# Kernel optimization log

Measured on AMD Instinct MI355X. Metric: run time of the kernel, lower is better.

The kernel has to match this reference:

```python
import jax, jax.numpy as jnp
import numpy as np

N_NODES = 100000   # ntoken
D = 128            # ninp
N_EDGES = 1600000  # n_nodes * avg_degree(16)


def setup_inputs() -> dict:
    key = jax.random.key(0)
    k0, k1, k2, k3 = jax.random.split(key, 4)
    # nn.Embedding weight, xavier_normal_ init; row 0 is padding_idx -> zeros
    emb = jax.random.normal(k0, (N_NODES, D), jnp.float32) * np.float32(np.sqrt(2.0 / (N_NODES + D)))
    emb = emb.at[0].set(0.0)
    # GCNConv weights (glorot) and biases (zeros), as in torch_geometric defaults
    W1 = jax.random.normal(k1, (D, 2 * D), jnp.float32) * np.float32(np.sqrt(2.0 / (D + 2 * D)))
    b1 = jnp.zeros((2 * D,), jnp.float32)
    W2 = jax.random.normal(k2, (2 * D, D), jnp.float32) * np.float32(np.sqrt(2.0 / (2 * D + D)))
    b2 = jnp.zeros((D,), jnp.float32)
    edge_index = jax.random.randint(k3, (2, N_EDGES), 0, N_NODES, dtype=jnp.int64)
    return {"emb": emb, "W1": W1, "b1": b1, "W2": W2, "b2": b2, "edge_index": edge_index}


def gcn_conv(x, W, b, src, dst, n):
    """torch_geometric GCNConv: add self-loops, sym deg^{-1/2} norm, edge_weight=1."""
    h = x @ W  # [n, out]
    loop = jnp.arange(n, dtype=src.dtype)
    src2 = jnp.concatenate([src, loop])
    dst2 = jnp.concatenate([dst, loop])
    # degree computed at destination (col) including self-loops
    deg = jax.ops.segment_sum(jnp.ones_like(src2, dtype=h.dtype), dst2, num_segments=n)
    dinv = jnp.where(deg > 0, jax.lax.rsqrt(deg), 0.0)
    norm = dinv[src2] * dinv[dst2]  # [E+n]
    msg = h[src2] * norm[:, None]   # gather + scale (memory-bound)
    out = jax.ops.segment_sum(msg, dst2, num_segments=n)  # scatter-add
    return out + b


def reference(emb, W1, b1, W2, b2, edge_index):
    src, dst = edge_index[0], edge_index[1]
    n = emb.shape[0]
    h = gcn_conv(emb, W1, b1, src, dst, n)   # [N, 2D]; dropout = identity (eval)
    out = gcn_conv(h, W2, b2, src, dst, n)   # [N, D]
    return out
```

## Files before the change

### kernel.cpp

```cpp
#include <hip/hip_runtime.h>

static constexpr int D = 128;
static constexpr int CAP = 64;
static constexpr int NSLICE = 8;

typedef __attribute__((ext_vector_type(8))) short bf16x8;
typedef __attribute__((ext_vector_type(4))) float f32x4;

__device__ inline unsigned bf16rne(float f) {
  unsigned u = __float_as_uint(f);
  return (u + 0x7FFFu + ((u >> 16) & 1u)) >> 16;
}

__global__ __launch_bounds__(256) void k_fill(const int* __restrict__ src,
                                              const int* __restrict__ dst,
                                              int* __restrict__ cnt,
                                              int* __restrict__ ell, int e, int n) {
  const int slice = blockIdx.x % NSLICE;
  const int chunk = blockIdx.x / NSLICE;
  const int lo = (int)((long long)n * slice / NSLICE);
  const int hi = (int)((long long)n * (slice + 1) / NSLICE);
  const int cbase = chunk * 4096;

  #pragma unroll
  for (int i = 0; i < 4; ++i) {
    int idx = cbase + i * 1024 + (int)threadIdx.x * 4;
    if (idx + 4 <= e) {
      int4 d4 = *(const int4*)(dst + idx);
      int4 s4 = *(const int4*)(src + idx);
      if (d4.x >= lo && d4.x < hi) { int p = atomicAdd(&cnt[d4.x], 1); if (p < CAP) ell[(size_t)d4.x * CAP + p] = s4.x; }
      if (d4.y >= lo && d4.y < hi) { int p = atomicAdd(&cnt[d4.y], 1); if (p < CAP) ell[(size_t)d4.y * CAP + p] = s4.y; }
      if (d4.z >= lo && d4.z < hi) { int p = atomicAdd(&cnt[d4.z], 1); if (p < CAP) ell[(size_t)d4.z * CAP + p] = s4.z; }
      if (d4.w >= lo && d4.w < hi) { int p = atomicAdd(&cnt[d4.w], 1); if (p < CAP) ell[(size_t)d4.w * CAP + p] = s4.w; }
    } else {
      for (int k = idx; k < e && k < idx + 4; ++k) {
        int s = src[k], d = dst[k];
        if (d >= lo && d < hi) { int p = atomicAdd(&cnt[d], 1); if (p < CAP) ell[(size_t)d * CAP + p] = s; }
      }
    }
  }
}

__global__ void k_cvt(const float4* __restrict__ in, uint2* __restrict__ out, int n4) {
  int i = blockIdx.x * blockDim.x + threadIdx.x;
  if (i >= n4) return;
  float4 v = in[i];
  uint2 r;
  r.x = bf16rne(v.x) | (bf16rne(v.y) << 16);
  r.y = bf16rne(v.z) | (bf16rne(v.w) << 16);
  out[i] = r;
}

__global__ void k_w1w2(const float* __restrict__ W1, const float* __restrict__ W2,
                       const float* __restrict__ b1, float* __restrict__ W,
                       float* __restrict__ c2) {
  int r = blockIdx.x, c = threadIdx.x;
  float acc = 0.f;
  for (int k = 0; k < 256; ++k) acc = fmaf(W1[r * 256 + k], W2[k * D + c], acc);
  W[r * D + c] = acc;
  if (r == 0) {
    float a2 = 0.f;
    for (int k = 0; k < 256; ++k) a2 = fmaf(b1[k], W2[k * D + c], a2);
    c2[c] = a2;
  }
}

__global__ void k_pack(const float* __restrict__ Wc, uint4* __restrict__ Wp) {
  int t = blockIdx.x * blockDim.x + threadIdx.x;
  if (t >= 2048) return;
  int l = t & 63, g = t >> 6;
  int ct = g >> 2, ks = g & 3;
  int col = ct * 16 + (l & 15);
  int k0 = ks * 32 + (l >> 4) * 8;
  unsigned r[4];
  #pragma unroll
  for (int jj = 0; jj < 4; ++jj) {
    unsigned lo = bf16rne(Wc[(size_t)(k0 + 2 * jj) * D + col]);
    unsigned hi = bf16rne(Wc[(size_t)(k0 + 2 * jj + 1) * D + col]);
    r[jj] = lo | (hi << 16);
  }
  Wp[t] = make_uint4(r[0], r[1], r[2], r[3]);
}

template<bool AOUT>
__global__ __launch_bounds__(256) void k_agg16(const uint2* __restrict__ x,
                                               const int* __restrict__ cnt,
                                               const int* __restrict__ ell,
                                               uint2* __restrict__ y,
                                               float* __restrict__ aout, int n) {
  int t = blockIdx.x * blockDim.x + threadIdx.x;
  int node = t >> 5, lane = t & 31;
  if (node >= n) return;
  int deg = cnt[node];
  float dd = rsqrtf(1.0f + (float)deg);
  int m = deg < CAP ? deg : CAP;
  const int* row = ell + (size_t)node * CAP;

  uint2 q = x[(size_t)node * 32 + lane];
  float4 acc;
  acc.x = __uint_as_float(q.x << 16) * dd;
  acc.y = __uint_as_float(q.x & 0xFFFF0000u) * dd;
  acc.z = __uint_as_float(q.y << 16) * dd;
  acc.w = __uint_as_float(q.y & 0xFFFF0000u) * dd;
  float ws = 0.f;

#define ACC4(Q, W)                                                         \
  acc.x = fmaf(__uint_as_float((Q).x << 16), (W), acc.x);                  \
  acc.y = fmaf(__uint_as_float((Q).x & 0xFFFF0000u), (W), acc.y);          \
  acc.z = fmaf(__uint_as_float((Q).y << 16), (W), acc.z);                  \
  acc.w = fmaf(__uint_as_float((Q).y & 0xFFFF0000u), (W), acc.w)

  int j = 0;
  for (; j + 8 <= m; j += 8) {
    int4 i0 = *(const int4*)(row + j);
    int4 i1 = *(const int4*)(row + j + 4);
    uint2 q0 = x[(size_t)i0.x * 32 + lane];
    uint2 q1 = x[(size_t)i0.y * 32 + lane];
    uint2 q2 = x[(size_t)i0.z * 32 + lane];
    uint2 q3 = x[(size_t)i0.w * 32 + lane];
    uint2 q4 = x[(size_t)i1.x * 32 + lane];
    uint2 q5 = x[(size_t)i1.y * 32 + lane];
    uint2 q6 = x[(size_t)i1.z * 32 + lane];
    uint2 q7 = x[(size_t)i1.w * 32 + lane];
    float w0 = rsqrtf(1.0f + (float)cnt[i0.x]);
    float w1 = rsqrtf(1.0f + (float)cnt[i0.y]);
    float w2 = rsqrtf(1.0f + (float)cnt[i0.z]);
    float w3 = rsqrtf(1.0f + (float)cnt[i0.w]);
    float w4 = rsqrtf(1.0f + (float)cnt[i1.x]);
    float w5 = rsqrtf(1.0f + (float)cnt[i1.y]);
    float w6 = rsqrtf(1.0f + (float)cnt[i1.z]);
    float w7 = rsqrtf(1.0f + (float)cnt[i1.w]);
    if (AOUT) ws += w0 + w1 + w2 + w3 + w4 + w5 + w6 + w7;
    ACC4(q0, w0); ACC4(q1, w1); ACC4(q2, w2); ACC4(q3, w3);
    ACC4(q4, w4); ACC4(q5, w5); ACC4(q6, w6); ACC4(q7, w7);
  }
  for (; j < m; ++j) {
    int s0 = row[j];
    uint2 q0 = x[(size_t)s0 * 32 + lane];
    float w0 = rsqrtf(1.0f + (float)cnt[s0]);
    if (AOUT) ws += w0;
    ACC4(q0, w0);
  }
#undef ACC4

  uint2 o;
  o.x = bf16rne(acc.x * dd) | (bf16rne(acc.y * dd) << 16);
  o.y = bf16rne(acc.z * dd) | (bf16rne(acc.w * dd) << 16);
  y[(size_t)node * 32 + lane] = o;
  if (AOUT && lane == 0) aout[node] = dd * (dd + ws);
}

__global__ __launch_bounds__(256) void k_gemm_mfma(const ushort* __restrict__ X,
                                                   const uint4* __restrict__ Wp,
                                                   const float* __restrict__ c2,
                                                   const float* __restrict__ b2,
                                                   const float* __restrict__ a,
                                                   float* __restrict__ Y, int n) {
  const int wv = threadIdx.x >> 6;
  const int l = threadIdx.x & 63;
  const int row0 = blockIdx.x * 64 + wv * 16;
  const int rA = row0 + (l & 15);
  const int kb = l >> 4;

  bf16x8 afr[4];
  #pragma unroll
  for (int ks = 0; ks < 4; ++ks) {
    bf16x8 z = 0;
    afr[ks] = (rA < n) ? *reinterpret_cast<const bf16x8*>(X + (size_t)rA * D + ks * 32 + kb * 8) : z;
  }

  float ar[4];
  #pragma unroll
  for (int r = 0; r < 4; ++r) {
    int row = row0 + kb * 4 + r;
    ar[r] = (row < n) ? a[row] : 0.f;
  }

  #pragma unroll
  for (int ct = 0; ct < 8; ++ct) {
    f32x4 acc = {0.f, 0.f, 0.f, 0.f};
    #pragma unroll
    for (int ks = 0; ks < 4; ++ks) {
      bf16x8 bfr = *reinterpret_cast<const bf16x8*>(Wp + (size_t)(ct * 4 + ks) * 64 + l);
      acc = __builtin_amdgcn_mfma_f32_16x16x32_bf16(afr[ks], bfr, acc, 0, 0, 0);
    }
    int col = ct * 16 + (l & 15);
    float cb = c2[col], bb = b2[col];
    #pragma unroll
    for (int r = 0; r < 4; ++r) {
      int row = row0 + kb * 4 + r;
      if (row < n) Y[(size_t)row * D + col] = acc[r] + ar[r] * cb + bb;
    }
  }
}

extern "C" void kernel_launch(void* const* d_in, const int* in_sizes, int n_in,
                              void* d_out, int out_size, void* d_ws, size_t ws_size,
                              hipStream_t stream) {
  const float* emb = (const float*)d_in[0];
  const float* W1  = (const float*)d_in[1];
  const float* b1  = (const float*)d_in[2];
  const float* W2  = (const float*)d_in[3];
  const float* b2  = (const float*)d_in[4];
  const int*   ei  = (const int*)d_in[5];

  const int n = in_sizes[0] / D;
  const int e = in_sizes[5] / 2;
  const int* src = ei;
  const int* dst = ei + e;

  const int B = 256;

  char* ws = (char*)d_ws;
  size_t off = 0;
  auto alloc = [&](size_t bytes) { void* p = ws + off; off = (off + bytes + 255) & ~(size_t)255; return p; };
  int*   cnt = (int*)  alloc((size_t)n * 4);
  int*   ell = (int*)  alloc((size_t)n * CAP * 4);
  float* Wc  = (float*)alloc((size_t)D * D * 4);
  uint4* Wp  = (uint4*)alloc(2048 * 16);
  float* c2  = (float*)alloc((size_t)D * 4);
  float* av  = (float*)alloc((size_t)n * 4);
  uint2* E16 = (uint2*)alloc((size_t)n * 32 * 8);
  uint2* S16 = (uint2*)alloc((size_t)n * 32 * 8);
  uint2* S2  = (uint2*)alloc((size_t)n * 32 * 8);
  float* out = (float*)d_out;

  (void)hipMemsetAsync(cnt, 0, (size_t)n * 4, stream);
  {
    int nchunk = (e + 4095) / 4096;
    k_fill<<<nchunk * NSLICE, B, 0, stream>>>(src, dst, cnt, ell, e, n);
  }

  {
    int n4 = n * 32;
    k_cvt<<<(n4 + B - 1) / B, B, 0, stream>>>((const float4*)emb, E16, n4);
  }

  k_w1w2<<<D, D, 0, stream>>>(W1, W2, b1, Wc, c2);
  k_pack<<<8, B, 0, stream>>>(Wc, Wp);

  {
    long long t = (long long)n * 32;
    k_agg16<false><<<(int)((t + B - 1) / B), B, 0, stream>>>(E16, cnt, ell, S16, nullptr, n);
  }
  {
    long long t = (long long)n * 32;
    k_agg16<true><<<(int)((t + B - 1) / B), B, 0, stream>>>(S16, cnt, ell, S2, av, n);
  }
  {
    int nblk = (n + 63) / 64;
    k_gemm_mfma<<<nblk, B, 0, stream>>>((const ushort*)S2, Wp, c2, b2, av, out, n);
  }
}
```

Baseline: 268.8 us.

## Bucket edges by destination slice in LDS and fuse prep kernels

Replaces the sliced ELL fill, which read every edge once per slice (8x), with a two-pass scheme. One pass bins each edge into per-slice queues in shared memory and writes them out as packed (local dst, src) words. A second kernel fills the ELL rows from each slice's queue. The bf16 conversion, W1·W2 product/packing and bias precompute are folded into the same launch, removing several kernel launches and the intermediate Wc buffer. Risks: bucket overflow drops edges if a chunk exceeds BCAP per slice, the 17-bit src packing caps node counts, and the extra queue traffic costs memory bandwidth.

```diff
diff --git a/kernel.cpp b/kernel.cpp
--- a/kernel.cpp
+++ b/kernel.cpp
@@ -3,6 +3,8 @@
 static constexpr int D = 128;
 static constexpr int CAP = 64;
 static constexpr int NSLICE = 8;
+static constexpr int BCAP = 768;
+static constexpr int CHUNK = 4096;
 
 typedef __attribute__((ext_vector_type(8))) short bf16x8;
 typedef __attribute__((ext_vector_type(4))) float f32x4;
@@ -12,74 +14,129 @@
   return (u + 0x7FFFu + ((u >> 16) & 1u)) >> 16;
 }
 
-__global__ __launch_bounds__(256) void k_fill(const int* __restrict__ src,
-                                              const int* __restrict__ dst,
-                                              int* __restrict__ cnt,
-                                              int* __restrict__ ell, int e, int n) {
+__global__ __launch_bounds__(256) void k_prep(
+    const int* __restrict__ src, const int* __restrict__ dst,
+    const float4* __restrict__ emb, uint2* __restrict__ E16,
+    const float* __restrict__ W1, const float* __restrict__ W2,
+    const float* __restrict__ b1, uint4* __restrict__ Wp, float* __restrict__ c2,
+    unsigned* __restrict__ queue, int* __restrict__ qtail,
+    int e, int q, int qcap, int nchunk, int ncvt, int n4) {
+  const int bid = blockIdx.x;
+  const int tid = threadIdx.x;
+
+  if (bid < nchunk) {
+    __shared__ unsigned buck[NSLICE][BCAP];
+    __shared__ int bcnt[NSLICE];
+    __shared__ int gbase[NSLICE];
+    if (tid < NSLICE) bcnt[tid] = 0;
+    __syncthreads();
+    const int base = bid * CHUNK;
+    #pragma unroll
+    for (int i = 0; i < 4; ++i) {
+      int idx = base + i * 1024 + tid * 4;
+      if (idx + 4 <= e) {
+        int4 d4 = *(const int4*)(dst + idx);
+        int4 s4 = *(const int4*)(src + idx);
+        { int d = d4.x, s = s4.x; int sl = d / q; int p = atomicAdd(&bcnt[sl], 1);
+          if (p < BCAP) buck[sl][p] = ((unsigned)(d - sl * q) << 17) | (unsigned)s; }
+        { int d = d4.y, s = s4.y; int sl = d / q; int p = atomicAdd(&bcnt[sl], 1);
+          if (p < BCAP) buck[sl][p] = ((unsigned)(d - sl * q) << 17) | (unsigned)s; }
+        { int d = d4.z, s = s4.z; int sl = d / q; int p = atomicAdd(&bcnt[sl], 1);
+          if (p < BCAP) buck[sl][p] = ((unsigned)(d - sl * q) << 17) | (unsigned)s; }
+        { int d = d4.w, s = s4.w; int sl = d / q; int p = atomicAdd(&bcnt[sl], 1);
+          if (p < BCAP) buck[sl][p] = ((unsigned)(d - sl * q) << 17) | (unsigned)s; }
+      } else {
+        for (int k = idx; k < e && k < idx + 4; ++k) {
+          int d = dst[k], s = src[k]; int sl = d / q; int p = atomicAdd(&bcnt[sl], 1);
+          if (p < BCAP) buck[sl][p] = ((unsigned)(d - sl * q) << 17) | (unsigned)s;
+        }
+      }
+    }
+    __syncthreads();
+    if (tid < NSLICE) {
+      int c = bcnt[tid] < BCAP ? bcnt[tid] : BCAP;
+      bcnt[tid] = c;
+      gbase[tid] = atomicAdd(&qtail[tid], c);
+    }
+    __syncthreads();
+    for (int s = 0; s < NSLICE; ++s) {
+      int cs = bcnt[s], gb = gbase[s];
+      unsigned* qs = queue + (size_t)s * qcap;
+      for (int i2 = tid; i2 < cs; i2 += 256) {
+        int pos = gb + i2;
+        if (pos < qcap) __builtin_nontemporal_store(buck[s][i2], qs + pos);
+      }
+    }
+  } else if (bid < nchunk + ncvt) {
+    int i0 = (bid - nchunk) * 1024 + tid;
+    #pragma unroll
+    for (int k = 0; k < 4; ++k) {
+      int i = i0 + k * 256;
+      if (i < n4) {
+        float4 v = emb[i];
+        uint2 r;
+        r.x = bf16rne(v.x) | (bf16rne(v.y) << 16);
+        r.y = bf16rne(v.z) | (bf16rne(v.w) << 16);
+        E16[i] = r;
+      }
+    }
+  } else {
+    int cb = bid - nchunk - ncvt;
+    if (cb < 8) {
+      int t = cb * 256 + tid;
+      int l = t & 63, g = t >> 6;
+      int ct = g >> 2, ks = g & 3;
+      int col = ct * 16 + (l & 15);
+      int k0 = ks * 32 + (l >> 4) * 8;
+      unsigned r[4];
+      #pragma unroll
+      for (int jj = 0; jj < 4; ++jj) {
+        float lo = 0.f, hi = 0.f;
+        for (int m = 0; m < 256; ++m) {
+          float w2v = W2[(size_t)m * D + col];
+          lo = fmaf(W1[(size_t)(k0 + 2 * jj) * 256 + m], w2v, lo);
+          hi = fmaf(W1[(size_t)(k0 + 2 * jj + 1) * 256 + m], w2v, hi);
+        }
+        r[jj] = bf16rne(lo) | (bf16rne(hi) << 16);
+      }
+      Wp[t] = make_uint4(r[0], r[1], r[2], r[3]);
+    } else if (tid < D) {
+      float a2 = 0.f;
+      for (int m = 0; m < 256; ++m) a2 = fmaf(b1[m], W2[(size_t)m * D + tid], a2);
+      c2[tid] = a2;
+    }
+  }
+}
+
+__global__ __launch_bounds__(256) void k_fillB(const unsigned* __restrict__ queue,
+                                               const int* __restrict__ qtail,
+                                               int* __restrict__ cnt,
+                                               int* __restrict__ ell, int q, int qcap) {
   const int slice = blockIdx.x % NSLICE;
   const int chunk = blockIdx.x / NSLICE;
-  const int lo = (int)((long long)n * slice / NSLICE);
-  const int hi = (int)((long long)n * (slice + 1) / NSLICE);
-  const int cbase = chunk * 4096;
-
-  #pragma unroll
-  for (int i = 0; i < 4; ++i) {
-    int idx = cbase + i * 1024 + (int)threadIdx.x * 4;
-    if (idx + 4 <= e) {
-      int4 d4 = *(const int4*)(dst + idx);
-      int4 s4 = *(const int4*)(src + idx);
-      if (d4.x >= lo && d4.x < hi) { int p = atomicAdd(&cnt[d4.x], 1); if (p < CAP) ell[(size_t)d4.x * CAP + p] = s4.x; }
-      if (d4.y >= lo && d4.y < hi) { int p = atomicAdd(&cnt[d4.y], 1); if (p < CAP) ell[(size_t)d4.y * CAP + p] = s4.y; }
-      if (d4.z >= lo && d4.z < hi) { int p = atomicAdd(&cnt[d4.z], 1); if (p < CAP) ell[(size_t)d4.z * CAP + p] = s4.z; }
-      if (d4.w >= lo && d4.w < hi) { int p = atomicAdd(&cnt[d4.w], 1); if (p < CAP) ell[(size_t)d4.w * CAP + p] = s4.w; }
+  int qlen = qtail[slice]; if (qlen > qcap) qlen = qcap;
+  const unsigned* qs = queue + (size_t)slice * qcap;
+  const int dbase = slice * q;
+  const int stride = (gridDim.x / NSLICE) * 256 * 4;
+
+  for (int i = chunk * 1024 + (int)threadIdx.x * 4; i < qlen; i += stride) {
+    if (i + 4 <= qlen) {
+      uint4 e4 = *(const uint4*)(qs + i);
+      { unsigned en = e4.x; int d = dbase + (int)(en >> 17); int s = (int)(en & 0x1FFFFu);
+        int p = atomicAdd(&cnt[d], 1); if (p < CAP) ell[(size_t)d * CAP + p] = s; }
+      { unsigned en = e4.y; int d = dbase + (int)(en >> 17); int s = (int)(en & 0x1FFFFu);
+        int p = atomicAdd(&cnt[d], 1); if (p < CAP) ell[(size_t)d * CAP + p] = s; }
+      { unsigned en = e4.z; int d = dbase + (int)(en >> 17); int s = (int)(en & 0x1FFFFu);
+        int p = atomicAdd(&cnt[d], 1); if (p < CAP) ell[(size_t)d * CAP + p] = s; }
+      { unsigned en = e4.w; int d = dbase + (int)(en >> 17); int s = (int)(en & 0x1FFFFu);
+        int p = atomicAdd(&cnt[d], 1); if (p < CAP) ell[(size_t)d * CAP + p] = s; }
     } else {
-      for (int k = idx; k < e && k < idx + 4; ++k) {
-        int s = src[k], d = dst[k];
-        if (d >= lo && d < hi) { int p = atomicAdd(&cnt[d], 1); if (p < CAP) ell[(size_t)d * CAP + p] = s; }
-      }
-    }
-  }
-}
-
-__global__ void k_cvt(const float4* __restrict__ in, uint2* __restrict__ out, int n4) {
-  int i = blockIdx.x * blockDim.x + threadIdx.x;
-  if (i >= n4) return;
-  float4 v = in[i];
-  uint2 r;
-  r.x = bf16rne(v.x) | (bf16rne(v.y) << 16);
-  r.y = bf16rne(v.z) | (bf16rne(v.w) << 16);
-  out[i] = r;
-}
-
-__global__ void k_w1w2(const float* __restrict__ W1, const float* __restrict__ W2,
-                       const float* __restrict__ b1, float* __restrict__ W,
-                       float* __restrict__ c2) {
-  int r = blockIdx.x, c = threadIdx.x;
-  float acc = 0.f;
-  for (int k = 0; k < 256; ++k) acc = fmaf(W1[r * 256 + k], W2[k * D + c], acc);
-  W[r * D + c] = acc;
-  if (r == 0) {
-    float a2 = 0.f;
-    for (int k = 0; k < 256; ++k) a2 = fmaf(b1[k], W2[k * D + c], a2);
-    c2[c] = a2;
-  }
-}
-
-__global__ void k_pack(const float* __restrict__ Wc, uint4* __restrict__ Wp) {
-  int t = blockIdx.x * blockDim.x + threadIdx.x;
-  if (t >= 2048) return;
-  int l = t & 63, g = t >> 6;
-  int ct = g >> 2, ks = g & 3;
-  int col = ct * 16 + (l & 15);
-  int k0 = ks * 32 + (l >> 4) * 8;
-  unsigned r[4];
-  #pragma unroll
-  for (int jj = 0; jj < 4; ++jj) {
-    unsigned lo = bf16rne(Wc[(size_t)(k0 + 2 * jj) * D + col]);
-    unsigned hi = bf16rne(Wc[(size_t)(k0 + 2 * jj + 1) * D + col]);
-    r[jj] = lo | (hi << 16);
-  }
-  Wp[t] = make_uint4(r[0], r[1], r[2], r[3]);
+      for (int k = i; k < qlen; ++k) {
+        unsigned en = qs[k]; int d = dbase + (int)(en >> 17); int s = (int)(en & 0x1FFFFu);
+        int p = atomicAdd(&cnt[d], 1); if (p < CAP) ell[(size_t)d * CAP + p] = s;
+      }
+    }
+  }
 }
 
 template<bool AOUT>
@@ -96,12 +153,12 @@
   int m = deg < CAP ? deg : CAP;
   const int* row = ell + (size_t)node * CAP;
 
-  uint2 q = x[(size_t)node * 32 + lane];
+  uint2 qv = x[(size_t)node * 32 + lane];
   float4 acc;
-  acc.x = __uint_as_float(q.x << 16) * dd;
-  acc.y = __uint_as_float(q.x & 0xFFFF0000u) * dd;
-  acc.z = __uint_as_float(q.y << 16) * dd;
-  acc.w = __uint_as_float(q.y & 0xFFFF0000u) * dd;
+  acc.x = __uint_as_float(qv.x << 16) * dd;
+  acc.y = __uint_as_float(qv.x & 0xFFFF0000u) * dd;
+  acc.z = __uint_as_float(qv.y << 16) * dd;
+  acc.w = __uint_as_float(qv.y & 0xFFFF0000u) * dd;
   float ws = 0.f;
 
 #define ACC4(Q, W)                                                         \
@@ -210,34 +267,32 @@
   const int* dst = ei + e;
 
   const int B = 256;
+  const int q = (n + NSLICE - 1) / NSLICE;
+  const int qcap = ((e / NSLICE + 8192) + 3) & ~3;
+  const int nchunk = (e + CHUNK - 1) / CHUNK;
+  const int n4 = n * 32;
+  const int ncvt = (n4 + 1023) / 1024;
 
   char* ws = (char*)d_ws;
   size_t off = 0;
   auto alloc = [&](size_t bytes) { void* p = ws + off; off = (off + bytes + 255) & ~(size_t)255; return p; };
-  int*   cnt = (int*)  alloc((size_t)n * 4);
-  int*   ell = (int*)  alloc((size_t)n * CAP * 4);
-  float* Wc  = (float*)alloc((size_t)D * D * 4);
-  uint4* Wp  = (uint4*)alloc(2048 * 16);
-  float* c2  = (float*)alloc((size_t)D * 4);
-  float* av  = (float*)alloc((size_t)n * 4);
-  uint2* E16 = (uint2*)alloc((size_t)n * 32 * 8);
-  uint2* S16 = (uint2*)alloc((size_t)n * 32 * 8);
-  uint2* S2  = (uint2*)alloc((size_t)n * 32 * 8);
-  float* out = (float*)d_out;
-
-  (void)hipMemsetAsync(cnt, 0, (size_t)n * 4, stream);
-  {
-    int nchunk = (e + 4095) / 4096;
-    k_fill<<<nchunk * NSLICE, B, 0, stream>>>(src, dst, cnt, ell, e, n);
-  }
-
-  {
-    int n4 = n * 32;
-    k_cvt<<<(n4 + B - 1) / B, B, 0, stream>>>((const float4*)emb, E16, n4);
-  }
-
-  k_w1w2<<<D, D, 0, stream>>>(W1, W2, b1, Wc, c2);
-  k_pack<<<8, B, 0, stream>>>(Wc, Wp);
+  int*      cnt   = (int*)     alloc((size_t)(n + 64) * 4);
+  int*      qtail = cnt + n;
+  int*      ell   = (int*)     alloc((size_t)n * CAP * 4);
+  unsigned* queue = (unsigned*)alloc((size_t)NSLICE * qcap * 4);
+  uint4*    Wp    = (uint4*)   alloc(2048 * 16);
+  float*    c2    = (float*)   alloc((size_t)D * 4);
+  float*    av    = (float*)   alloc((size_t)n * 4);
+  uint2*    E16   = (uint2*)   alloc((size_t)n * 32 * 8);
+  uint2*    S16   = (uint2*)   alloc((size_t)n * 32 * 8);
+  uint2*    S2    = (uint2*)   alloc((size_t)n * 32 * 8);
+  float*    out   = (float*)d_out;
+
+  (void)hipMemsetAsync(cnt, 0, (size_t)(n + 64) * 4, stream);
+  k_prep<<<nchunk + ncvt + 9, B, 0, stream>>>(src, dst, (const float4*)emb, E16,
+                                              W1, W2, b1, Wp, c2, queue, qtail,
+                                              e, q, qcap, nchunk, ncvt, n4);
+  k_fillB<<<48 * NSLICE, B, 0, stream>>>(queue, qtail, cnt, ell, q, qcap);
 
   {
     long long t = (long long)n * 32;
```

Result: slower. 280.0 us (+4.1%).

## Move fused weight GEMM before aggregation and co-launch it with ELL fill

Applied to the files above, without the earlier changes.

The fused W1·W2 projection is now applied to the embeddings first, which relies on linearity: A(A·X·W1+b1)W2 equals A·A·(X·W1W2) + A·1·b1W2. The bias terms are folded into the aggregation epilogues: c2 is added after the first aggregation and b2 after the second, which writes fp32 output directly. This removes the separate bf16 conversion kernel, the final GEMM pass and the per-node coefficient vector. The GEMM blocks share one launch with the edge-fill blocks so the two run concurrently, and weight prep collapses into one kernel. Fill loads use nontemporal hints. The trade-off is that the bf16 rounding now happens in a different place.

```diff
diff --git a/kernel.cpp b/kernel.cpp
--- a/kernel.cpp
+++ b/kernel.cpp
@@ -3,91 +3,128 @@
 static constexpr int D = 128;
 static constexpr int CAP = 64;
 static constexpr int NSLICE = 8;
+static constexpr int CHUNK = 4096;
 
 typedef __attribute__((ext_vector_type(8))) short bf16x8;
 typedef __attribute__((ext_vector_type(4))) float f32x4;
+typedef __attribute__((ext_vector_type(4))) int iv4;
 
 __device__ inline unsigned bf16rne(float f) {
   unsigned u = __float_as_uint(f);
   return (u + 0x7FFFu + ((u >> 16) & 1u)) >> 16;
 }
 
-__global__ __launch_bounds__(256) void k_fill(const int* __restrict__ src,
-                                              const int* __restrict__ dst,
-                                              int* __restrict__ cnt,
-                                              int* __restrict__ ell, int e, int n) {
-  const int slice = blockIdx.x % NSLICE;
-  const int chunk = blockIdx.x / NSLICE;
-  const int lo = (int)((long long)n * slice / NSLICE);
-  const int hi = (int)((long long)n * (slice + 1) / NSLICE);
-  const int cbase = chunk * 4096;
-
-  #pragma unroll
-  for (int i = 0; i < 4; ++i) {
-    int idx = cbase + i * 1024 + (int)threadIdx.x * 4;
-    if (idx + 4 <= e) {
-      int4 d4 = *(const int4*)(dst + idx);
-      int4 s4 = *(const int4*)(src + idx);
-      if (d4.x >= lo && d4.x < hi) { int p = atomicAdd(&cnt[d4.x], 1); if (p < CAP) ell[(size_t)d4.x * CAP + p] = s4.x; }
-      if (d4.y >= lo && d4.y < hi) { int p = atomicAdd(&cnt[d4.y], 1); if (p < CAP) ell[(size_t)d4.y * CAP + p] = s4.y; }
-      if (d4.z >= lo && d4.z < hi) { int p = atomicAdd(&cnt[d4.z], 1); if (p < CAP) ell[(size_t)d4.z * CAP + p] = s4.z; }
-      if (d4.w >= lo && d4.w < hi) { int p = atomicAdd(&cnt[d4.w], 1); if (p < CAP) ell[(size_t)d4.w * CAP + p] = s4.w; }
-    } else {
-      for (int k = idx; k < e && k < idx + 4; ++k) {
-        int s = src[k], d = dst[k];
-        if (d >= lo && d < hi) { int p = atomicAdd(&cnt[d], 1); if (p < CAP) ell[(size_t)d * CAP + p] = s; }
-      }
-    }
-  }
-}
-
-__global__ void k_cvt(const float4* __restrict__ in, uint2* __restrict__ out, int n4) {
-  int i = blockIdx.x * blockDim.x + threadIdx.x;
-  if (i >= n4) return;
-  float4 v = in[i];
-  uint2 r;
-  r.x = bf16rne(v.x) | (bf16rne(v.y) << 16);
-  r.y = bf16rne(v.z) | (bf16rne(v.w) << 16);
-  out[i] = r;
-}
-
-__global__ void k_w1w2(const float* __restrict__ W1, const float* __restrict__ W2,
-                       const float* __restrict__ b1, float* __restrict__ W,
-                       float* __restrict__ c2) {
-  int r = blockIdx.x, c = threadIdx.x;
-  float acc = 0.f;
-  for (int k = 0; k < 256; ++k) acc = fmaf(W1[r * 256 + k], W2[k * D + c], acc);
-  W[r * D + c] = acc;
-  if (r == 0) {
+__global__ __launch_bounds__(256) void k_wprep(const float* __restrict__ W1,
+                                               const float* __restrict__ W2,
+                                               const float* __restrict__ b1,
+                                               uint4* __restrict__ Wp,
+                                               float* __restrict__ c2) {
+  int cb = blockIdx.x;
+  int tid = threadIdx.x;
+  if (cb < 8) {
+    int t = cb * 256 + tid;
+    int l = t & 63, g = t >> 6;
+    int ct = g >> 2, ks = g & 3;
+    int col = ct * 16 + (l & 15);
+    int k0 = ks * 32 + (l >> 4) * 8;
+    unsigned r[4];
+    #pragma unroll
+    for (int jj = 0; jj < 4; ++jj) {
+      float lo = 0.f, hi = 0.f;
+      for (int m = 0; m < 256; ++m) {
+        float w2v = W2[(size_t)m * D + col];
+        lo = fmaf(W1[(size_t)(k0 + 2 * jj) * 256 + m], w2v, lo);
+        hi = fmaf(W1[(size_t)(k0 + 2 * jj + 1) * 256 + m], w2v, hi);
+      }
+      r[jj] = bf16rne(lo) | (bf16rne(hi) << 16);
+    }
+    Wp[t] = make_uint4(r[0], r[1], r[2], r[3]);
+  } else if (tid < D) {
     float a2 = 0.f;
-    for (int k = 0; k < 256; ++k) a2 = fmaf(b1[k], W2[k * D + c], a2);
-    c2[c] = a2;
-  }
-}
-
-__global__ void k_pack(const float* __restrict__ Wc, uint4* __restrict__ Wp) {
-  int t = blockIdx.x * blockDim.x + threadIdx.x;
-  if (t >= 2048) return;
-  int l = t & 63, g = t >> 6;
-  int ct = g >> 2, ks = g & 3;
-  int col = ct * 16 + (l & 15);
-  int k0 = ks * 32 + (l >> 4) * 8;
-  unsigned r[4];
-  #pragma unroll
-  for (int jj = 0; jj < 4; ++jj) {
-    unsigned lo = bf16rne(Wc[(size_t)(k0 + 2 * jj) * D + col]);
-    unsigned hi = bf16rne(Wc[(size_t)(k0 + 2 * jj + 1) * D + col]);
-    r[jj] = lo | (hi << 16);
-  }
-  Wp[t] = make_uint4(r[0], r[1], r[2], r[3]);
-}
-
-template<bool AOUT>
+    for (int m = 0; m < 256; ++m) a2 = fmaf(b1[m], W2[(size_t)m * D + tid], a2);
+    c2[tid] = a2;
+  }
+}
+
+__global__ __launch_bounds__(256) void k_combo(
+    const int* __restrict__ src, const int* __restrict__ dst,
+    int* __restrict__ cnt, int* __restrict__ ell,
+    const float4* __restrict__ emb4, const uint4* __restrict__ Wp,
+    ushort* __restrict__ G16, int e, int n, int fillblocks) {
+  const int bid = blockIdx.x;
+  const int tid = threadIdx.x;
+
+  if (bid < fillblocks) {
+    const int slice = bid % NSLICE;
+    const int chunk = bid / NSLICE;
+    const int lo = (int)((long long)n * slice / NSLICE);
+    const int hi = (int)((long long)n * (slice + 1) / NSLICE);
+    const int cbase = chunk * CHUNK;
+    #pragma unroll
+    for (int i = 0; i < 4; ++i) {
+      int idx = cbase + i * 1024 + tid * 4;
+      if (idx + 4 <= e) {
+        iv4 d4 = __builtin_nontemporal_load((const iv4*)(dst + idx));
+        iv4 s4 = __builtin_nontemporal_load((const iv4*)(src + idx));
+        if (d4.x >= lo && d4.x < hi) { int p = atomicAdd(&cnt[d4.x], 1); if (p < CAP) ell[(size_t)d4.x * CAP + p] = s4.x; }
+        if (d4.y >= lo && d4.y < hi) { int p = atomicAdd(&cnt[d4.y], 1); if (p < CAP) ell[(size_t)d4.y * CAP + p] = s4.y; }
+        if (d4.z >= lo && d4.z < hi) { int p = atomicAdd(&cnt[d4.z], 1); if (p < CAP) ell[(size_t)d4.z * CAP + p] = s4.z; }
+        if (d4.w >= lo && d4.w < hi) { int p = atomicAdd(&cnt[d4.w], 1); if (p < CAP) ell[(size_t)d4.w * CAP + p] = s4.w; }
+      } else {
+        for (int k = idx; k < e && k < idx + 4; ++k) {
+          int s = src[k], d = dst[k];
+          if (d >= lo && d < hi) { int p = atomicAdd(&cnt[d], 1); if (p < CAP) ell[(size_t)d * CAP + p] = s; }
+        }
+      }
+    }
+  } else {
+    const int gb = bid - fillblocks;
+    const int wv = tid >> 6;
+    const int l = tid & 63;
+    const int row0 = gb * 64 + wv * 16;
+    const int rA = row0 + (l & 15);
+    const int kb = l >> 4;
+
+    bf16x8 afr[4];
+    #pragma unroll
+    for (int ks = 0; ks < 4; ++ks) {
+      bf16x8 a = 0;
+      if (rA < n) {
+        float4 v0 = emb4[(size_t)rA * 32 + ks * 8 + kb * 2];
+        float4 v1 = emb4[(size_t)rA * 32 + ks * 8 + kb * 2 + 1];
+        a[0] = (short)bf16rne(v0.x); a[1] = (short)bf16rne(v0.y);
+        a[2] = (short)bf16rne(v0.z); a[3] = (short)bf16rne(v0.w);
+        a[4] = (short)bf16rne(v1.x); a[5] = (short)bf16rne(v1.y);
+        a[6] = (short)bf16rne(v1.z); a[7] = (short)bf16rne(v1.w);
+      }
+      afr[ks] = a;
+    }
+
+    #pragma unroll
+    for (int ct = 0; ct < 8; ++ct) {
+      f32x4 acc = {0.f, 0.f, 0.f, 0.f};
+      #pragma unroll
+      for (int ks = 0; ks < 4; ++ks) {
+        bf16x8 bfr = *reinterpret_cast<const bf16x8*>(Wp + (size_t)(ct * 4 + ks) * 64 + l);
+        acc = __builtin_amdgcn_mfma_f32_16x16x32_bf16(afr[ks], bfr, acc, 0, 0, 0);
+      }
+      int col = ct * 16 + (l & 15);
+      #pragma unroll
+      for (int r = 0; r < 4; ++r) {
+        int row = row0 + kb * 4 + r;
+        if (row < n) G16[(size_t)row * D + col] = (ushort)bf16rne(acc[r]);
+      }
+    }
+  }
+}
+
+template<bool OUT32>
 __global__ __launch_bounds__(256) void k_agg16(const uint2* __restrict__ x,
                                                const int* __restrict__ cnt,
                                                const int* __restrict__ ell,
-                                               uint2* __restrict__ y,
-                                               float* __restrict__ aout, int n) {
+                                               const float* __restrict__ addv,
+                                               uint2* __restrict__ y16,
+                                               float4* __restrict__ y32, int n) {
   int t = blockIdx.x * blockDim.x + threadIdx.x;
   int node = t >> 5, lane = t & 31;
   if (node >= n) return;
@@ -96,13 +133,12 @@
   int m = deg < CAP ? deg : CAP;
   const int* row = ell + (size_t)node * CAP;
 
-  uint2 q = x[(size_t)node * 32 + lane];
+  uint2 qv = x[(size_t)node * 32 + lane];
   float4 acc;
-  acc.x = __uint_as_float(q.x << 16) * dd;
-  acc.y = __uint_as_float(q.x & 0xFFFF0000u) * dd;
-  acc.z = __uint_as_float(q.y << 16) * dd;
-  acc.w = __uint_as_float(q.y & 0xFFFF0000u) * dd;
-  float ws = 0.f;
+  acc.x = __uint_as_float(qv.x << 16) * dd;
+  acc.y = __uint_as_float(qv.x & 0xFFFF0000u) * dd;
+  acc.z = __uint_as_float(qv.y << 16) * dd;
+  acc.w = __uint_as_float(qv.y & 0xFFFF0000u) * dd;
 
 #define ACC4(Q, W)                                                         \
   acc.x = fmaf(__uint_as_float((Q).x << 16), (W), acc.x);                  \
@@ -130,7 +166,6 @@
     float w5 = rsqrtf(1.0f + (float)cnt[i1.y]);
     float w6 = rsqrtf(1.0f + (float)cnt[i1.z]);
     float w7 = rsqrtf(1.0f + (float)cnt[i1.w]);
-    if (AOUT) ws += w0 + w1 + w2 + w3 + w4 + w5 + w6 + w7;
     ACC4(q0, w0); ACC4(q1, w1); ACC4(q2, w2); ACC4(q3, w3);
     ACC4(q4, w4); ACC4(q5, w5); ACC4(q6, w6); ACC4(q7, w7);
   }
@@ -138,59 +173,21 @@
     int s0 = row[j];
     uint2 q0 = x[(size_t)s0 * 32 + lane];
     float w0 = rsqrtf(1.0f + (float)cnt[s0]);
-    if (AOUT) ws += w0;
     ACC4(q0, w0);
   }
 #undef ACC4
 
-  uint2 o;
-  o.x = bf16rne(acc.x * dd) | (bf16rne(acc.y * dd) << 16);
-  o.y = bf16rne(acc.z * dd) | (bf16rne(acc.w * dd) << 16);
-  y[(size_t)node * 32 + lane] = o;
-  if (AOUT && lane == 0) aout[node] = dd * (dd + ws);
-}
-
-__global__ __launch_bounds__(256) void k_gemm_mfma(const ushort* __restrict__ X,
-                                                   const uint4* __restrict__ Wp,
-                                                   const float* __restrict__ c2,
-                                                   const float* __restrict__ b2,
-                                                   const float* __restrict__ a,
-                                                   float* __restrict__ Y, int n) {
-  const int wv = threadIdx.x >> 6;
-  const int l = threadIdx.x & 63;
-  const int row0 = blockIdx.x * 64 + wv * 16;
-  const int rA = row0 + (l & 15);
-  const int kb = l >> 4;
-
-  bf16x8 afr[4];
-  #pragma unroll
-  for (int ks = 0; ks < 4; ++ks) {
-    bf16x8 z = 0;
-    afr[ks] = (rA < n) ? *reinterpret_cast<const bf16x8*>(X + (size_t)rA * D + ks * 32 + kb * 8) : z;
-  }
-
-  float ar[4];
-  #pragma unroll
-  for (int r = 0; r < 4; ++r) {
-    int row = row0 + kb * 4 + r;
-    ar[r] = (row < n) ? a[row] : 0.f;
-  }
-
-  #pragma unroll
-  for (int ct = 0; ct < 8; ++ct) {
-    f32x4 acc = {0.f, 0.f, 0.f, 0.f};
-    #pragma unroll
-    for (int ks = 0; ks < 4; ++ks) {
-      bf16x8 bfr = *reinterpret_cast<const bf16x8*>(Wp + (size_t)(ct * 4 + ks) * 64 + l);
-      acc = __builtin_amdgcn_mfma_f32_16x16x32_bf16(afr[ks], bfr, acc, 0, 0, 0);
-    }
-    int col = ct * 16 + (l & 15);
-    float cb = c2[col], bb = b2[col];
-    #pragma unroll
-    for (int r = 0; r < 4; ++r) {
-      int row = row0 + kb * 4 + r;
-      if (row < n) Y[(size_t)row * D + col] = acc[r] + ar[r] * cb + bb;
-    }
+  float4 b = ((const float4*)addv)[lane];
+  float4 o;
+  o.x = fmaf(acc.x, dd, b.x); o.y = fmaf(acc.y, dd, b.y);
+  o.z = fmaf(acc.z, dd, b.z); o.w = fmaf(acc.w, dd, b.w);
+  if (OUT32) {
+    y32[(size_t)node * 32 + lane] = o;
+  } else {
+    uint2 p;
+    p.x = bf16rne(o.x) | (bf16rne(o.y) << 16);
+    p.y = bf16rne(o.z) | (bf16rne(o.w) << 16);
+    y16[(size_t)node * 32 + lane] = p;
   }
 }
 
@@ -210,45 +207,36 @@
   const int* dst = ei + e;
 
   const int B = 256;
+  const int nchunk = (e + CHUNK - 1) / CHUNK;
+  const int fillblocks = nchunk * NSLICE;
+  const int gemmblocks = (n + 63) / 64;
 
   char* ws = (char*)d_ws;
   size_t off = 0;
   auto alloc = [&](size_t bytes) { void* p = ws + off; off = (off + bytes + 255) & ~(size_t)255; return p; };
-  int*   cnt = (int*)  alloc((size_t)n * 4);
-  int*   ell = (int*)  alloc((size_t)n * CAP * 4);
-  float* Wc  = (float*)alloc((size_t)D * D * 4);
-  uint4* Wp  = (uint4*)alloc(2048 * 16);
-  float* c2  = (float*)alloc((size_t)D * 4);
-  float* av  = (float*)alloc((size_t)n * 4);
-  uint2* E16 = (uint2*)alloc((size_t)n * 32 * 8);
-  uint2* S16 = (uint2*)alloc((size_t)n * 32 * 8);
-  uint2* S2  = (uint2*)alloc((size_t)n * 32 * 8);
-  float* out = (float*)d_out;
+  int*    cnt = (int*)   alloc((size_t)n * 4);
+  int*    ell = (int*)   alloc((size_t)n * CAP * 4);
+  uint4*  Wp  = (uint4*) alloc(2048 * 16);
+  float*  c2  = (float*) alloc((size_t)D * 4);
+  ushort* G16 = (ushort*)alloc((size_t)n * D * 2);
+  ushort* H16 = (ushort*)alloc((size_t)n * D * 2);
+  float*  out = (float*)d_out;
+
+  k_wprep<<<9, B, 0, stream>>>(W1, W2, b1, Wp, c2);
 
   (void)hipMemsetAsync(cnt, 0, (size_t)n * 4, stream);
-  {
-    int nchunk = (e + 4095) / 4096;
-    k_fill<<<nchunk * NSLICE, B, 0, stream>>>(src, dst, cnt, ell, e, n);
-  }
-
-  {
-    int n4 = n * 32;
-    k_cvt<<<(n4 + B - 1) / B, B, 0, stream>>>((const float4*)emb, E16, n4);
-  }
-
-  k_w1w2<<<D, D, 0, stream>>>(W1, W2, b1, Wc, c2);
-  k_pack<<<8, B, 0, stream>>>(Wc, Wp);
+  k_combo<<<fillblocks + gemmblocks, B, 0, stream>>>(src, dst, cnt, ell,
+                                                     (const float4*)emb, Wp, G16,
+                                                     e, n, fillblocks);
 
   {
     long long t = (long long)n * 32;
-    k_agg16<false><<<(int)((t + B - 1) / B), B, 0, stream>>>(E16, cnt, ell, S16, nullptr, n);
+    k_agg16<false><<<(int)((t + B - 1) / B), B, 0, stream>>>(
+        (const uint2*)G16, cnt, ell, c2, (uint2*)H16, nullptr, n);
   }
   {
     long long t = (long long)n * 32;
-    k_agg16<true><<<(int)((t + B - 1) / B), B, 0, stream>>>(S16, cnt, ell, S2, av, n);
-  }
-  {
-    int nblk = (n + 63) / 64;
-    k_gemm_mfma<<<nblk, B, 0, stream>>>((const ushort*)S2, Wp, c2, b2, av, out, n);
-  }
-}
+    k_agg16<true><<<(int)((t + B - 1) / B), B, 0, stream>>>(
+        (const uint2*)H16, cnt, ell, b2, nullptr, (float4*)out, n);
+  }
+}
```

New measurement: 270.9 us. About the same (+0.8%).
